# Performance work log

Measured on AMD Instinct MI355X. Metric: run time of the kernel, lower is better.

Reference implementation:

```python
import jax, jax.numpy as jnp
import numpy as np

D_MODEL = 768
N_HEADS = 12
HEAD_DIM = D_MODEL // N_HEADS


def setup_inputs() -> dict:
    key = jax.random.key(0)
    ks = jax.random.split(key, 9)
    B, S = 4, 2048
    std = 1.0 / np.sqrt(D_MODEL)
    x = jax.random.normal(ks[0], (B, S, D_MODEL), dtype=jnp.float32)
    Wq = jax.random.normal(ks[1], (D_MODEL, D_MODEL), dtype=jnp.float32) * std
    bq = jnp.zeros((D_MODEL,), dtype=jnp.float32)
    Wk = jax.random.normal(ks[2], (D_MODEL, D_MODEL), dtype=jnp.float32) * std
    bk = jnp.zeros((D_MODEL,), dtype=jnp.float32)
    Wv = jax.random.normal(ks[3], (D_MODEL, D_MODEL), dtype=jnp.float32) * std
    bv = jnp.zeros((D_MODEL,), dtype=jnp.float32)
    Wo = jax.random.normal(ks[4], (D_MODEL, D_MODEL), dtype=jnp.float32) * std
    bo = jnp.zeros((D_MODEL,), dtype=jnp.float32)
    return {"x": x, "Wq": Wq, "bq": bq, "Wk": Wk, "bk": bk,
            "Wv": Wv, "bv": bv, "Wo": Wo, "bo": bo}


def reference(x, Wq, bq, Wk, bk, Wv, bv, Wo, bo):
    B, S, D = x.shape
    H, Hd = N_HEADS, HEAD_DIM
    # QKV projections (torch Linear: y = x @ W^T + b; here W stored as [in,out])
    q = (x @ Wq + bq).reshape(B, S, H, Hd).transpose(0, 2, 1, 3)  # [B,H,S,Hd]
    k = (x @ Wk + bk).reshape(B, S, H, Hd).transpose(0, 2, 1, 3)
    v = (x @ Wv + bv).reshape(B, S, H, Hd).transpose(0, 2, 1, 3)
    scale = 1.0 / jnp.sqrt(jnp.asarray(Hd, dtype=x.dtype))
    scores = jnp.einsum('bhqd,bhkd->bhqk', q, k) * scale  # [B,H,S,S]
    causal = jnp.tril(jnp.ones((S, S), dtype=bool))
    scores = jnp.where(causal, scores, -jnp.inf)
    attn = jax.nn.softmax(scores, axis=-1)
    ctx = jnp.einsum('bhqk,bhkd->bhqd', attn, v)  # [B,H,S,Hd]
    ctx = ctx.transpose(0, 2, 1, 3).reshape(B, S, D)
    return ctx @ Wo + bo
```

## Files before the change

### kernel.cpp

```cpp
#include <hip/hip_runtime.h>
#include <stdint.h>

#define DM    768
#define NH    12
#define HD    64
#define BATCH 4
#define SEQ   2048
#define NTOK  (BATCH*SEQ)
#define NKT   12

typedef unsigned int   u32;
typedef unsigned short u16;
using bf16x8 = __attribute__((ext_vector_type(8))) short;
using f32x4  = __attribute__((ext_vector_type(4))) float;

#define QSCALE 0.18033688011112042f

__device__ __forceinline__ u16 f2bf(float f) {
    u32 u = __float_as_uint(f);
    u = (u + 0x7FFFu + ((u >> 16) & 1u)) >> 16;
    return (u16)u;
}

__device__ __forceinline__ u32 pkbf(float a, float b) {
    u32 r;
    asm("v_cvt_pk_bf16_f32 %0, %1, %2" : "=v"(r) : "v"(a), "v"(b));
    return r;
}

template <int N>
__device__ __forceinline__ void waitvm() {
    if constexpr (N == 0)      asm volatile("s_waitcnt vmcnt(0)" ::: "memory");
    else if constexpr (N == 5) asm volatile("s_waitcnt vmcnt(5)" ::: "memory");
    else if constexpr (N == 8) asm volatile("s_waitcnt vmcnt(8)" ::: "memory");
    else if constexpr (N == 9) asm volatile("s_waitcnt vmcnt(9)" ::: "memory");
    else                       static_assert(N == 0 || N == 5 || N == 8 || N == 9, "add literal");
}

__device__ __forceinline__ void gload_lds16(const void* gptr, void* ldsptr) {
    __builtin_amdgcn_global_load_lds(
        (__attribute__((address_space(1))) const u32*)gptr,
        (__attribute__((address_space(3))) u32*)ldsptr, 16, 0, 0);
}

__device__ __forceinline__ float vmax4(f32x4 v) {
    return fmaxf(fmaxf(v[0], v[1]), fmaxf(v[2], v[3]));
}

__global__ void cvt_x(const float* __restrict__ x, u16* __restrict__ xb, int n4) {
    int i = blockIdx.x * blockDim.x + threadIdx.x;
    if (i >= n4) return;
    float4 v = ((const float4*)x)[i];
    ushort4 o;
    o.x = f2bf(v.x); o.y = f2bf(v.y); o.z = f2bf(v.z); o.w = f2bf(v.w);
    ((ushort4*)xb)[i] = o;
}

__global__ void transpose_w4(const float* __restrict__ q, const float* __restrict__ k,
                             const float* __restrict__ v, const float* __restrict__ o,
                             u16* __restrict__ Wt, u16* __restrict__ Wto) {
    __shared__ float tile[32][33];
    int z = blockIdx.z;
    const float* W = (z == 0) ? q : (z == 1) ? k : (z == 2) ? v : o;
    u16* D = (z < 3) ? (Wt + (size_t)z * DM * DM) : Wto;
    int tx = threadIdx.x, ty = threadIdx.y;
    int x0 = blockIdx.x * 32, y0 = blockIdx.y * 32;
    #pragma unroll
    for (int i = 0; i < 32; i += 8)
        tile[ty + i][tx] = W[(size_t)(y0 + ty + i) * DM + x0 + tx];
    __syncthreads();
    #pragma unroll
    for (int i = 0; i < 32; i += 8)
        D[(size_t)(x0 + ty + i) * DM + y0 + tx] = f2bf(tile[tx][ty + i]);
}

template <int MODE>
__global__ __launch_bounds__(512, 2)
void gemm_pipe(const u16* __restrict__ A, const u16* __restrict__ Bt,
               const float* __restrict__ b0, const float* __restrict__ b1,
               const float* __restrict__ b2,
               u16* __restrict__ Qo, u16* __restrict__ Ko, u16* __restrict__ Vto,
               float* __restrict__ Out)
{
    constexpr int BM = (MODE == 0) ? 256 : 128;
    constexpr int BN = (MODE == 0) ? 288 : 192;
    constexpr int MF = 4;
    constexpr int NF = (MODE == 0) ? 9 : 3;
    constexpr int AL = BM / 64;
    constexpr int BFULL = (MODE == 0) ? 4 : 3;

    __shared__ u16 As[2][BM][64];
    __shared__ u16 Bs[2][BN][64];

    const int t = threadIdx.x;
    const int w = t >> 6, l = t & 63;
    const int l15 = l & 15, lg = l >> 4;
    const int m0 = blockIdx.x * BM;
    const int n0 = blockIdx.y * BN;
    const int waveM = ((MODE == 0) ? (w >> 1) : (w >> 2)) * 64;
    const int waveN = (MODE == 0) ? (w & 1) * 144 : (w & 3) * 48;

    f32x4 zf = {0.f, 0.f, 0.f, 0.f};
    f32x4 acc[MF][NF];
    #pragma unroll
    for (int i = 0; i < MF; ++i)
        #pragma unroll
        for (int j = 0; j < NF; ++j) acc[i][j] = zf;

    const u16* Arow0 = A  + (size_t)m0 * DM;
    const u16* Brow0 = Bt + (size_t)n0 * DM;

    auto stage = [&](int d, int k0) {
        #pragma unroll
        for (int i = 0; i < AL; ++i) {
            int f = i * 512 + t;
            int row = f >> 3, c = f & 7;
            int gc = c ^ (row & 7);
            gload_lds16(Arow0 + (size_t)row * DM + k0 + gc * 8, &As[d][row][c * 8]);
        }
        #pragma unroll
        for (int i = 0; i < BFULL; ++i) {
            int f = i * 512 + t;
            int row = f >> 3, c = f & 7;
            int gc = c ^ (row & 7);
            gload_lds16(Brow0 + (size_t)row * DM + k0 + gc * 8, &Bs[d][row][c * 8]);
        }
        if constexpr (MODE == 0) {
            if (t < 256) {
                int f = 2048 + t;
                int row = f >> 3, c = f & 7;
                int gc = c ^ (row & 7);
                gload_lds16(Brow0 + (size_t)row * DM + k0 + gc * 8, &Bs[d][row][c * 8]);
            }
        }
    };
    auto wait_tile = [&]() {
        if constexpr (MODE == 0) {
            if (w < 4) waitvm<9>(); else waitvm<8>();
        } else {
            waitvm<5>();
        }
    };
    auto phase = [&](int d, int kk) {
        const int ch = ((kk * 4 + lg) ^ (l15 & 7)) * 8;
        bf16x8 af[MF], bfr[NF];
        #pragma unroll
        for (int m = 0; m < MF; ++m)
            af[m] = *(const bf16x8*)&As[d][waveM + m * 16 + l15][ch];
        #pragma unroll
        for (int n = 0; n < NF; ++n)
            bfr[n] = *(const bf16x8*)&Bs[d][waveN + n * 16 + l15][ch];
        __builtin_amdgcn_s_setprio(1);
        #pragma unroll
        for (int m = 0; m < MF; ++m)
            #pragma unroll
            for (int n = 0; n < NF; ++n)
                acc[m][n] = __builtin_amdgcn_mfma_f32_16x16x32_bf16(af[m], bfr[n], acc[m][n], 0, 0, 0);
        __builtin_amdgcn_s_setprio(0);
    };

    stage(0, 0);
    stage(1, 64);

    for (int tt = 0; tt < NKT - 1; ++tt) {
        const int c = tt & 1;
        wait_tile();
        __builtin_amdgcn_s_barrier();
        __builtin_amdgcn_sched_barrier(0);
        phase(c, 0);
        phase(c, 1);
        __builtin_amdgcn_sched_barrier(0);
        __builtin_amdgcn_s_barrier();
        __builtin_amdgcn_sched_barrier(0);
        if (tt + 2 < NKT) stage(c, (tt + 2) * 64);
    }
    {
        waitvm<0>();
        __builtin_amdgcn_s_barrier();
        __builtin_amdgcn_sched_barrier(0);
        phase((NKT - 1) & 1, 0);
        phase((NKT - 1) & 1, 1);
    }

    if (MODE == 1) {
        #pragma unroll
        for (int m = 0; m < MF; ++m) {
            int grow = m0 + waveM + m * 16 + lg * 4;
            #pragma unroll
            for (int n = 0; n < NF; ++n) {
                int gcol = n0 + waveN + n * 16 + l15;
                float bias = b0[gcol];
                #pragma unroll
                for (int r = 0; r < 4; ++r)
                    Out[(size_t)(grow + r) * DM + gcol] = acc[m][n][r] + bias;
            }
        }
    } else {
        #pragma unroll
        for (int m = 0; m < MF; ++m) {
            int grow = m0 + waveM + m * 16 + lg * 4;
            int bb = grow >> 11, ss = grow & 2047;
            #pragma unroll
            for (int n = 0; n < NF; ++n) {
                int nstart = n0 + waveN + n * 16;
                int which = nstart / DM;
                int cbase = nstart - which * DM + l15;
                int h = cbase >> 6, hd = cbase & 63;
                if (which == 0) {
                    float bias = b0[cbase];
                    #pragma unroll
                    for (int r = 0; r < 4; ++r)
                        Qo[(((size_t)bb * NH + h) * SEQ + (ss + r)) * HD + hd] =
                            f2bf((acc[m][n][r] + bias) * QSCALE);
                } else if (which == 1) {
                    float bias = b1[cbase];
                    #pragma unroll
                    for (int r = 0; r < 4; ++r)
                        Ko[(((size_t)bb * NH + h) * SEQ + (ss + r)) * HD + hd] =
                            f2bf(acc[m][n][r] + bias);
                } else {
                    float bias = b2[cbase];
                    u32 lo = pkbf(acc[m][n][0] + bias, acc[m][n][1] + bias);
                    u32 hi = pkbf(acc[m][n][2] + bias, acc[m][n][3] + bias);
                    *(int2*)&Vto[(((size_t)bb * NH + h) * HD + hd) * SEQ + ss] =
                        make_int2((int)lo, (int)hi);
                }
            }
        }
    }
}

__global__ __launch_bounds__(512, 3)
void attn_fwd(const u16* __restrict__ Q, const u16* __restrict__ K_,
              const u16* __restrict__ Vt, u16* __restrict__ ctx)
{
    __shared__ u16 Ks[2][64][64];
    __shared__ u16 Vs[2][64][64];

    const int t = threadIdx.x, w = t >> 6, l = t & 63;
    const int l15 = l & 15, lg = l >> 4;
    const int sw = l15 & 7;
    const int bx = blockIdx.x;
    const int ord = bx / 48;
    const int bh  = bx - ord * 48;
    const int q8  = 7 - ord;
    const int b = bh / NH, h = bh - b * NH;
    const int wrow0 = q8 * 256 + w * 32;
    const int jmax = 4 * q8 + 3;

    const u16* Qp0 = Q + ((size_t)bh * SEQ + wrow0 + l15) * HD;
    const u16* Qp1 = Qp0 + 16 * HD;
    bf16x8 qf00 = *(const bf16x8*)(Qp0 + lg * 8);
    bf16x8 qf01 = *(const bf16x8*)(Qp0 + 32 + lg * 8);
    bf16x8 qf10 = *(const bf16x8*)(Qp1 + lg * 8);
    bf16x8 qf11 = *(const bf16x8*)(Qp1 + 32 + lg * 8);

    f32x4 zf = {0.f, 0.f, 0.f, 0.f};
    f32x4 acc0[4], acc1[4];
    #pragma unroll
    for (int d = 0; d < 4; ++d) { acc0[d] = zf; acc1[d] = zf; }
    float mi0 = -INFINITY, li0 = 0.f;
    float mi1 = -INFINITY, li1 = 0.f;

    const u16* Kbh = K_ + (size_t)bh * SEQ * HD;
    const u16* Vbh = Vt + (size_t)bh * HD * SEQ;
    const int row = t >> 3, c = t & 7;
    const int cw = (c ^ (row & 7)) * 8;

    {
        int4 kr = *(const int4*)(Kbh + (size_t)row * HD + c * 8);
        int4 vr = *(const int4*)(Vbh + (size_t)row * SEQ + c * 8);
        *(int4*)&Ks[0][row][cw] = kr;
        *(int4*)&Vs[0][row][cw] = vr;
    }
    __syncthreads();

    for (int jt = 0; jt <= jmax; ++jt) {
        const int cur = jt & 1;
        const int j0 = jt << 6;
        int4 kn, vn;
        if (jt < jmax) {
            int j1 = j0 + 64;
            kn = *(const int4*)(Kbh + (size_t)(j1 + row) * HD + c * 8);
            vn = *(const int4*)(Vbh + (size_t)row * SEQ + j1 + c * 8);
        }
        if (j0 <= wrow0 + 31) {
            const u16 (*Kc)[64] = Ks[cur];
            const u16 (*Vc)[64] = Vs[cur];
            f32x4 s0[4], s1[4];
            __builtin_amdgcn_s_setprio(1);
            #pragma unroll
            for (int nt = 0; nt < 4; ++nt) {
                bf16x8 kf0 = *(const bf16x8*)&Kc[nt * 16 + l15][(lg ^ sw) * 8];
                bf16x8 kf1 = *(const bf16x8*)&Kc[nt * 16 + l15][((4 + lg) ^ sw) * 8];
                f32x4 a = zf;
                a = __builtin_amdgcn_mfma_f32_16x16x32_bf16(kf0, qf00, a, 0, 0, 0);
                a = __builtin_amdgcn_mfma_f32_16x16x32_bf16(kf1, qf01, a, 0, 0, 0);
                s0[nt] = a;
                f32x4 c2 = zf;
                c2 = __builtin_amdgcn_mfma_f32_16x16x32_bf16(kf0, qf10, c2, 0, 0, 0);
                c2 = __builtin_amdgcn_mfma_f32_16x16x32_bf16(kf1, qf11, c2, 0, 0, 0);
                s1[nt] = c2;
            }
            __builtin_amdgcn_s_setprio(0);
            if (j0 + 63 > wrow0) {
                #pragma unroll
                for (int nt = 0; nt < 4; ++nt) {
                    int kb = j0 + nt * 16 + lg * 4;
                    #pragma unroll
                    for (int r = 0; r < 4; ++r) {
                        if (kb + r > wrow0 + l15)      s0[nt][r] = -INFINITY;
                        if (kb + r > wrow0 + 16 + l15) s1[nt][r] = -INFINITY;
                    }
                }
            }
            float pm0 = fmaxf(fmaxf(vmax4(s0[0]), vmax4(s0[1])), fmaxf(vmax4(s0[2]), vmax4(s0[3])));
            float pm1 = fmaxf(fmaxf(vmax4(s1[0]), vmax4(s1[1])), fmaxf(vmax4(s1[2]), vmax4(s1[3])));
            pm0 = fmaxf(pm0, __shfl_xor(pm0, 16)); pm0 = fmaxf(pm0, __shfl_xor(pm0, 32));
            pm1 = fmaxf(pm1, __shfl_xor(pm1, 16)); pm1 = fmaxf(pm1, __shfl_xor(pm1, 32));
            if (!__all((pm0 <= mi0 + 8.f) && (pm1 <= mi1 + 8.f))) {
                float mn0 = fmaxf(mi0, pm0), mn1 = fmaxf(mi1, pm1);
                float so0 = __builtin_amdgcn_exp2f(mi0 - mn0);
                float so1 = __builtin_amdgcn_exp2f(mi1 - mn1);
                mi0 = mn0; mi1 = mn1;
                li0 *= so0; li1 *= so1;
                float a0 = __shfl(so0, lg * 4 + 0), a1 = __shfl(so0, lg * 4 + 1);
                float a2 = __shfl(so0, lg * 4 + 2), a3 = __shfl(so0, lg * 4 + 3);
                float b0_ = __shfl(so1, lg * 4 + 0), b1_ = __shfl(so1, lg * 4 + 1);
                float b2_ = __shfl(so1, lg * 4 + 2), b3_ = __shfl(so1, lg * 4 + 3);
                #pragma unroll
                for (int d = 0; d < 4; ++d) {
                    acc0[d][0] *= a0;  acc0[d][1] *= a1;  acc0[d][2] *= a2;  acc0[d][3] *= a3;
                    acc1[d][0] *= b0_; acc1[d][1] *= b1_; acc1[d][2] *= b2_; acc1[d][3] *= b3_;
                }
            }
            u32 dwa[8], dwb[8];
            float rs0 = 0.f, rs1 = 0.f;
            #pragma unroll
            for (int nt = 0; nt < 4; ++nt) {
                float p0 = __builtin_amdgcn_exp2f(s0[nt][0] - mi0);
                float p1 = __builtin_amdgcn_exp2f(s0[nt][1] - mi0);
                float p2 = __builtin_amdgcn_exp2f(s0[nt][2] - mi0);
                float p3 = __builtin_amdgcn_exp2f(s0[nt][3] - mi0);
                rs0 += (p0 + p1) + (p2 + p3);
                dwa[nt * 2] = pkbf(p0, p1); dwa[nt * 2 + 1] = pkbf(p2, p3);
                float q0 = __builtin_amdgcn_exp2f(s1[nt][0] - mi1);
                float q1 = __builtin_amdgcn_exp2f(s1[nt][1] - mi1);
                float q2 = __builtin_amdgcn_exp2f(s1[nt][2] - mi1);
                float q3 = __builtin_amdgcn_exp2f(s1[nt][3] - mi1);
                rs1 += (q0 + q1) + (q2 + q3);
                dwb[nt * 2] = pkbf(q0, q1); dwb[nt * 2 + 1] = pkbf(q2, q3);
            }
            bf16x8 pa00 = __builtin_bit_cast(bf16x8, make_int4((int)dwa[0], (int)dwa[1], (int)dwa[2], (int)dwa[3]));
            bf16x8 pa01 = __builtin_bit_cast(bf16x8, make_int4((int)dwa[4], (int)dwa[5], (int)dwa[6], (int)dwa[7]));
            bf16x8 pa10 = __builtin_bit_cast(bf16x8, make_int4((int)dwb[0], (int)dwb[1], (int)dwb[2], (int)dwb[3]));
            bf16x8 pa11 = __builtin_bit_cast(bf16x8, make_int4((int)dwb[4], (int)dwb[5], (int)dwb[6], (int)dwb[7]));
            const int o4 = (lg & 1) * 4, c0 = lg >> 1;
            __builtin_amdgcn_s_setprio(1);
            #pragma unroll
            for (int d = 0; d < 4; ++d) {
                const u16* vrow = Vc[d * 16 + l15];
                int2 v0 = *(const int2*)(vrow + (((c0 + 0) ^ sw) * 8 + o4));
                int2 v1 = *(const int2*)(vrow + (((c0 + 2) ^ sw) * 8 + o4));
                int2 v2 = *(const int2*)(vrow + (((c0 + 4) ^ sw) * 8 + o4));
                int2 v3 = *(const int2*)(vrow + (((c0 + 6) ^ sw) * 8 + o4));
                bf16x8 vf0 = __builtin_bit_cast(bf16x8, make_int4(v0.x, v0.y, v1.x, v1.y));
                bf16x8 vf1 = __builtin_bit_cast(bf16x8, make_int4(v2.x, v2.y, v3.x, v3.y));
                acc0[d] = __builtin_amdgcn_mfma_f32_16x16x32_bf16(pa00, vf0, acc0[d], 0, 0, 0);
                acc0[d] = __builtin_amdgcn_mfma_f32_16x16x32_bf16(pa01, vf1, acc0[d], 0, 0, 0);
                acc1[d] = __builtin_amdgcn_mfma_f32_16x16x32_bf16(pa10, vf0, acc1[d], 0, 0, 0);
                acc1[d] = __builtin_amdgcn_mfma_f32_16x16x32_bf16(pa11, vf1, acc1[d], 0, 0, 0);
            }
            __builtin_amdgcn_s_setprio(0);
            rs0 += __shfl_xor(rs0, 16); rs0 += __shfl_xor(rs0, 32);
            rs1 += __shfl_xor(rs1, 16); rs1 += __shfl_xor(rs1, 32);
            li0 += rs0; li1 += rs1;
        }
        if (jt < jmax) {
            *(int4*)&Ks[cur ^ 1][row][cw] = kn;
            *(int4*)&Vs[cur ^ 1][row][cw] = vn;
        }
        __syncthreads();
    }

    float e00 = 1.0f / __shfl(li0, lg * 4 + 0), e01 = 1.0f / __shfl(li0, lg * 4 + 1);
    float e02 = 1.0f / __shfl(li0, lg * 4 + 2), e03 = 1.0f / __shfl(li0, lg * 4 + 3);
    float e10 = 1.0f / __shfl(li1, lg * 4 + 0), e11 = 1.0f / __shfl(li1, lg * 4 + 1);
    float e12 = 1.0f / __shfl(li1, lg * 4 + 2), e13 = 1.0f / __shfl(li1, lg * 4 + 3);
    #pragma unroll
    for (int r = 0; r < 4; ++r) {
        float f0 = (r == 0) ? e00 : (r == 1) ? e01 : (r == 2) ? e02 : e03;
        float f1 = (r == 0) ? e10 : (r == 1) ? e11 : (r == 2) ? e12 : e13;
        int s0r = wrow0 + lg * 4 + r;
        size_t base0 = ((size_t)b * SEQ + s0r) * DM + h * HD;
        size_t base1 = ((size_t)b * SEQ + s0r + 16) * DM + h * HD;
        #pragma unroll
        for (int d = 0; d < 4; ++d) {
            ctx[base0 + d * 16 + l15] = f2bf(acc0[d][r] * f0);
            ctx[base1 + d * 16 + l15] = f2bf(acc1[d][r] * f1);
        }
    }
}

extern "C" void kernel_launch(void* const* d_in, const int* in_sizes, int n_in,
                              void* d_out, int out_size, void* d_ws, size_t ws_size,
                              hipStream_t stream) {
    const float* x  = (const float*)d_in[0];
    const float* Wq = (const float*)d_in[1];
    const float* bq = (const float*)d_in[2];
    const float* Wk = (const float*)d_in[3];
    const float* bk = (const float*)d_in[4];
    const float* Wv = (const float*)d_in[5];
    const float* bv = (const float*)d_in[6];
    const float* Wo = (const float*)d_in[7];
    const float* bo = (const float*)d_in[8];
    float* out = (float*)d_out;

    char* ws = (char*)d_ws;
    u16* xb  = (u16*)(ws);
    u16* Wt  = (u16*)(ws + 12582912);
    u16* Wto = (u16*)(ws + 16121856);
    u16* Qw  = (u16*)(ws + 17301504);
    u16* Kw  = (u16*)(ws + 29884416);
    u16* Vtw = (u16*)(ws + 42467328);
    u16* ctx = (u16*)(ws + 55050240);

    cvt_x<<<6144, 256, 0, stream>>>(x, xb, NTOK * DM / 4);
    dim3 tb(32, 8), tg4(24, 24, 4);
    transpose_w4<<<tg4, tb, 0, stream>>>(Wq, Wk, Wv, Wo, Wt, Wto);

    dim3 g2(32, 8);
    gemm_pipe<0><<<g2, 512, 0, stream>>>(xb, Wt, bq, bk, bv, Qw, Kw, Vtw, nullptr);
    attn_fwd<<<384, 512, 0, stream>>>(Qw, Kw, Vtw, ctx);
    dim3 g4(64, 4);
    gemm_pipe<1><<<g4, 512, 0, stream>>>(ctx, Wto, bo, nullptr, nullptr, nullptr, nullptr, nullptr, out);
}
```

Before: 135.0 us.

## Double attention KV tile to 128 keys per sync and raise launch bounds

The attention loop now stages 128 keys of K and V per iteration instead of 64. It processes them as two 64-key halves from the same shared buffers, which halves the number of block barriers and global-to-LDS prefetch rounds. The V layout becomes 64x128 with a matching swizzle. Launch bounds rise from 3 to 4 blocks per CU, which tightens the register budget. Shared memory per block doubles to 64KB, which may cap resident blocks below the requested 4 and risks spills or lower occupancy.

Result: slower. 152.3 us (+12.8%).

```diff
diff --git a/kernel.cpp b/kernel.cpp
--- a/kernel.cpp
+++ b/kernel.cpp
@@ -230,12 +230,12 @@
     }
 }
 
-__global__ __launch_bounds__(512, 3)
+__global__ __launch_bounds__(512, 4)
 void attn_fwd(const u16* __restrict__ Q, const u16* __restrict__ K_,
               const u16* __restrict__ Vt, u16* __restrict__ ctx)
 {
-    __shared__ u16 Ks[2][64][64];
-    __shared__ u16 Vs[2][64][64];
+    __shared__ u16 Ks[2][128][64];
+    __shared__ u16 Vs[2][64][128];
 
     const int t = threadIdx.x, w = t >> 6, l = t & 63;
     const int l15 = l & 15, lg = l >> 4;
@@ -246,7 +246,7 @@
     const int q8  = 7 - ord;
     const int b = bh / NH, h = bh - b * NH;
     const int wrow0 = q8 * 256 + w * 32;
-    const int jmax = 4 * q8 + 3;
+    const int niter = 2 * q8 + 2;
 
     const u16* Qp0 = Q + ((size_t)bh * SEQ + wrow0 + l15) * HD;
     const u16* Qp1 = Qp0 + 16 * HD;
@@ -264,121 +264,138 @@
 
     const u16* Kbh = K_ + (size_t)bh * SEQ * HD;
     const u16* Vbh = Vt + (size_t)bh * HD * SEQ;
-    const int row = t >> 3, c = t & 7;
-    const int cw = (c ^ (row & 7)) * 8;
+    const int rk = t >> 3, ck = t & 7;
+    const int rv = t >> 4, cv = t & 15;
+    const int kw0 = (ck ^ (rk & 7)) * 8;
+    const int kw1 = (ck ^ ((rk + 64) & 7)) * 8;
+    const int vw0 = ((cv ^ (rv & 7)) & 15) * 8;
+    const int vw1 = ((cv ^ ((rv + 32) & 7)) & 15) * 8;
 
     {
-        int4 kr = *(const int4*)(Kbh + (size_t)row * HD + c * 8);
-        int4 vr = *(const int4*)(Vbh + (size_t)row * SEQ + c * 8);
-        *(int4*)&Ks[0][row][cw] = kr;
-        *(int4*)&Vs[0][row][cw] = vr;
+        int4 k0r = *(const int4*)(Kbh + (size_t)rk * HD + ck * 8);
+        int4 k1r = *(const int4*)(Kbh + (size_t)(rk + 64) * HD + ck * 8);
+        int4 v0r = *(const int4*)(Vbh + (size_t)rv * SEQ + cv * 8);
+        int4 v1r = *(const int4*)(Vbh + (size_t)(rv + 32) * SEQ + cv * 8);
+        *(int4*)&Ks[0][rk][kw0]      = k0r;
+        *(int4*)&Ks[0][rk + 64][kw1] = k1r;
+        *(int4*)&Vs[0][rv][vw0]      = v0r;
+        *(int4*)&Vs[0][rv + 32][vw1] = v1r;
     }
     __syncthreads();
 
-    for (int jt = 0; jt <= jmax; ++jt) {
+    for (int jt = 0; jt < niter; ++jt) {
         const int cur = jt & 1;
-        const int j0 = jt << 6;
-        int4 kn, vn;
-        if (jt < jmax) {
-            int j1 = j0 + 64;
-            kn = *(const int4*)(Kbh + (size_t)(j1 + row) * HD + c * 8);
-            vn = *(const int4*)(Vbh + (size_t)row * SEQ + j1 + c * 8);
-        }
-        if (j0 <= wrow0 + 31) {
-            const u16 (*Kc)[64] = Ks[cur];
-            const u16 (*Vc)[64] = Vs[cur];
-            f32x4 s0[4], s1[4];
-            __builtin_amdgcn_s_setprio(1);
-            #pragma unroll
-            for (int nt = 0; nt < 4; ++nt) {
-                bf16x8 kf0 = *(const bf16x8*)&Kc[nt * 16 + l15][(lg ^ sw) * 8];
-                bf16x8 kf1 = *(const bf16x8*)&Kc[nt * 16 + l15][((4 + lg) ^ sw) * 8];
-                f32x4 a = zf;
-                a = __builtin_amdgcn_mfma_f32_16x16x32_bf16(kf0, qf00, a, 0, 0, 0);
-                a = __builtin_amdgcn_mfma_f32_16x16x32_bf16(kf1, qf01, a, 0, 0, 0);
-                s0[nt] = a;
-                f32x4 c2 = zf;
-                c2 = __builtin_amdgcn_mfma_f32_16x16x32_bf16(kf0, qf10, c2, 0, 0, 0);
-                c2 = __builtin_amdgcn_mfma_f32_16x16x32_bf16(kf1, qf11, c2, 0, 0, 0);
-                s1[nt] = c2;
-            }
-            __builtin_amdgcn_s_setprio(0);
-            if (j0 + 63 > wrow0) {
+        const int j0 = jt << 7;
+        int4 kn0, kn1, vn0, vn1;
+        if (jt < niter - 1) {
+            int j1 = j0 + 128;
+            kn0 = *(const int4*)(Kbh + (size_t)(j1 + rk) * HD + ck * 8);
+            kn1 = *(const int4*)(Kbh + (size_t)(j1 + rk + 64) * HD + ck * 8);
+            vn0 = *(const int4*)(Vbh + (size_t)rv * SEQ + j1 + cv * 8);
+            vn1 = *(const int4*)(Vbh + (size_t)(rv + 32) * SEQ + j1 + cv * 8);
+        }
+        const u16 (*Kc)[64]  = Ks[cur];
+        const u16 (*Vc)[128] = Vs[cur];
+        #pragma unroll
+        for (int hk = 0; hk < 2; ++hk) {
+            const int j0h = j0 + hk * 64;
+            if (j0h <= wrow0 + 31) {
+                f32x4 s0[4], s1[4];
+                __builtin_amdgcn_s_setprio(1);
                 #pragma unroll
                 for (int nt = 0; nt < 4; ++nt) {
-                    int kb = j0 + nt * 16 + lg * 4;
+                    const u16* krow = Kc[hk * 64 + nt * 16 + l15];
+                    bf16x8 kf0 = *(const bf16x8*)&krow[(lg ^ sw) * 8];
+                    bf16x8 kf1 = *(const bf16x8*)&krow[((4 + lg) ^ sw) * 8];
+                    f32x4 a = zf;
+                    a = __builtin_amdgcn_mfma_f32_16x16x32_bf16(kf0, qf00, a, 0, 0, 0);
+                    a = __builtin_amdgcn_mfma_f32_16x16x32_bf16(kf1, qf01, a, 0, 0, 0);
+                    s0[nt] = a;
+                    f32x4 c2 = zf;
+                    c2 = __builtin_amdgcn_mfma_f32_16x16x32_bf16(kf0, qf10, c2, 0, 0, 0);
+                    c2 = __builtin_amdgcn_mfma_f32_16x16x32_bf16(kf1, qf11, c2, 0, 0, 0);
+                    s1[nt] = c2;
+                }
+                __builtin_amdgcn_s_setprio(0);
+                if (j0h + 63 > wrow0) {
                     #pragma unroll
-                    for (int r = 0; r < 4; ++r) {
-                        if (kb + r > wrow0 + l15)      s0[nt][r] = -INFINITY;
-                        if (kb + r > wrow0 + 16 + l15) s1[nt][r] = -INFINITY;
+                    for (int nt = 0; nt < 4; ++nt) {
+                        int kb = j0h + nt * 16 + lg * 4;
+                        #pragma unroll
+                        for (int r = 0; r < 4; ++r) {
+                            if (kb + r > wrow0 + l15)      s0[nt][r] = -INFINITY;
+                            if (kb + r > wrow0 + 16 + l15) s1[nt][r] = -INFINITY;
+                        }
                     }
                 }
-            }
-            float pm0 = fmaxf(fmaxf(vmax4(s0[0]), vmax4(s0[1])), fmaxf(vmax4(s0[2]), vmax4(s0[3])));
-            float pm1 = fmaxf(fmaxf(vmax4(s1[0]), vmax4(s1[1])), fmaxf(vmax4(s1[2]), vmax4(s1[3])));
-            pm0 = fmaxf(pm0, __shfl_xor(pm0, 16)); pm0 = fmaxf(pm0, __shfl_xor(pm0, 32));
-            pm1 = fmaxf(pm1, __shfl_xor(pm1, 16)); pm1 = fmaxf(pm1, __shfl_xor(pm1, 32));
-            if (!__all((pm0 <= mi0 + 8.f) && (pm1 <= mi1 + 8.f))) {
-                float mn0 = fmaxf(mi0, pm0), mn1 = fmaxf(mi1, pm1);
-                float so0 = __builtin_amdgcn_exp2f(mi0 - mn0);
-                float so1 = __builtin_amdgcn_exp2f(mi1 - mn1);
-                mi0 = mn0; mi1 = mn1;
-                li0 *= so0; li1 *= so1;
-                float a0 = __shfl(so0, lg * 4 + 0), a1 = __shfl(so0, lg * 4 + 1);
-                float a2 = __shfl(so0, lg * 4 + 2), a3 = __shfl(so0, lg * 4 + 3);
-                float b0_ = __shfl(so1, lg * 4 + 0), b1_ = __shfl(so1, lg * 4 + 1);
-                float b2_ = __shfl(so1, lg * 4 + 2), b3_ = __shfl(so1, lg * 4 + 3);
+                float pm0 = fmaxf(fmaxf(vmax4(s0[0]), vmax4(s0[1])), fmaxf(vmax4(s0[2]), vmax4(s0[3])));
+                float pm1 = fmaxf(fmaxf(vmax4(s1[0]), vmax4(s1[1])), fmaxf(vmax4(s1[2]), vmax4(s1[3])));
+                pm0 = fmaxf(pm0, __shfl_xor(pm0, 16)); pm0 = fmaxf(pm0, __shfl_xor(pm0, 32));
+                pm1 = fmaxf(pm1, __shfl_xor(pm1, 16)); pm1 = fmaxf(pm1, __shfl_xor(pm1, 32));
+                if (!__all((pm0 <= mi0 + 8.f) && (pm1 <= mi1 + 8.f))) {
+                    float mn0 = fmaxf(mi0, pm0), mn1 = fmaxf(mi1, pm1);
+                    float so0 = __builtin_amdgcn_exp2f(mi0 - mn0);
+                    float so1 = __builtin_amdgcn_exp2f(mi1 - mn1);
+                    mi0 = mn0; mi1 = mn1;
+                    li0 *= so0; li1 *= so1;
+                    float a0 = __shfl(so0, lg * 4 + 0), a1 = __shfl(so0, lg * 4 + 1);
+                    float a2 = __shfl(so0, lg * 4 + 2), a3 = __shfl(so0, lg * 4 + 3);
+                    float b0_ = __shfl(so1, lg * 4 + 0), b1_ = __shfl(so1, lg * 4 + 1);
+                    float b2_ = __shfl(so1, lg * 4 + 2), b3_ = __shfl(so1, lg * 4 + 3);
+                    #pragma unroll
+                    for (int d = 0; d < 4; ++d) {
+                        acc0[d][0] *= a0;  acc0[d][1] *= a1;  acc0[d][2] *= a2;  acc0[d][3] *= a3;
+                        acc1[d][0] *= b0_; acc1[d][1] *= b1_; acc1[d][2] *= b2_; acc1[d][3] *= b3_;
+                    }
+                }
+                u32 dwa[8], dwb[8];
+                float rs0 = 0.f, rs1 = 0.f;
+                #pragma unroll
+                for (int nt = 0; nt < 4; ++nt) {
+                    float p0 = __builtin_amdgcn_exp2f(s0[nt][0] - mi0);
+                    float p1 = __builtin_amdgcn_exp2f(s0[nt][1] - mi0);
+                    float p2 = __builtin_amdgcn_exp2f(s0[nt][2] - mi0);
+                    float p3 = __builtin_amdgcn_exp2f(s0[nt][3] - mi0);
+                    rs0 += (p0 + p1) + (p2 + p3);
+                    dwa[nt * 2] = pkbf(p0, p1); dwa[nt * 2 + 1] = pkbf(p2, p3);
+                    float q0 = __builtin_amdgcn_exp2f(s1[nt][0] - mi1);
+                    float q1 = __builtin_amdgcn_exp2f(s1[nt][1] - mi1);
+                    float q2 = __builtin_amdgcn_exp2f(s1[nt][2] - mi1);
+                    float q3 = __builtin_amdgcn_exp2f(s1[nt][3] - mi1);
+                    rs1 += (q0 + q1) + (q2 + q3);
+                    dwb[nt * 2] = pkbf(q0, q1); dwb[nt * 2 + 1] = pkbf(q2, q3);
+                }
+                rs0 += __shfl_xor(rs0, 16); rs0 += __shfl_xor(rs0, 32);
+                rs1 += __shfl_xor(rs1, 16); rs1 += __shfl_xor(rs1, 32);
+                li0 += rs0; li1 += rs1;
+                bf16x8 pa00 = __builtin_bit_cast(bf16x8, make_int4((int)dwa[0], (int)dwa[1], (int)dwa[2], (int)dwa[3]));
+                bf16x8 pa01 = __builtin_bit_cast(bf16x8, make_int4((int)dwa[4], (int)dwa[5], (int)dwa[6], (int)dwa[7]));
+                bf16x8 pa10 = __builtin_bit_cast(bf16x8, make_int4((int)dwb[0], (int)dwb[1], (int)dwb[2], (int)dwb[3]));
+                bf16x8 pa11 = __builtin_bit_cast(bf16x8, make_int4((int)dwb[4], (int)dwb[5], (int)dwb[6], (int)dwb[7]));
+                const int o4 = (lg & 1) * 4, c0 = lg >> 1;
+                __builtin_amdgcn_s_setprio(1);
                 #pragma unroll
                 for (int d = 0; d < 4; ++d) {
-                    acc0[d][0] *= a0;  acc0[d][1] *= a1;  acc0[d][2] *= a2;  acc0[d][3] *= a3;
-                    acc1[d][0] *= b0_; acc1[d][1] *= b1_; acc1[d][2] *= b2_; acc1[d][3] *= b3_;
-                }
+                    const u16* vrow = Vc[d * 16 + l15] + hk * 64;
+                    int2 v0 = *(const int2*)(vrow + (((c0 + 0) ^ sw) * 8 + o4));
+                    int2 v1 = *(const int2*)(vrow + (((c0 + 2) ^ sw) * 8 + o4));
+                    int2 v2 = *(const int2*)(vrow + (((c0 + 4) ^ sw) * 8 + o4));
+                    int2 v3 = *(const int2*)(vrow + (((c0 + 6) ^ sw) * 8 + o4));
+                    bf16x8 vf0 = __builtin_bit_cast(bf16x8, make_int4(v0.x, v0.y, v1.x, v1.y));
+                    bf16x8 vf1 = __builtin_bit_cast(bf16x8, make_int4(v2.x, v2.y, v3.x, v3.y));
+                    acc0[d] = __builtin_amdgcn_mfma_f32_16x16x32_bf16(pa00, vf0, acc0[d], 0, 0, 0);
+                    acc0[d] = __builtin_amdgcn_mfma_f32_16x16x32_bf16(pa01, vf1, acc0[d], 0, 0, 0);
+                    acc1[d] = __builtin_amdgcn_mfma_f32_16x16x32_bf16(pa10, vf0, acc1[d], 0, 0, 0);
+                    acc1[d] = __builtin_amdgcn_mfma_f32_16x16x32_bf16(pa11, vf1, acc1[d], 0, 0, 0);
+                }
+                __builtin_amdgcn_s_setprio(0);
             }
-            u32 dwa[8], dwb[8];
-            float rs0 = 0.f, rs1 = 0.f;
-            #pragma unroll
-            for (int nt = 0; nt < 4; ++nt) {
-                float p0 = __builtin_amdgcn_exp2f(s0[nt][0] - mi0);
-                float p1 = __builtin_amdgcn_exp2f(s0[nt][1] - mi0);
-                float p2 = __builtin_amdgcn_exp2f(s0[nt][2] - mi0);
-                float p3 = __builtin_amdgcn_exp2f(s0[nt][3] - mi0);
-                rs0 += (p0 + p1) + (p2 + p3);
-                dwa[nt * 2] = pkbf(p0, p1); dwa[nt * 2 + 1] = pkbf(p2, p3);
-                float q0 = __builtin_amdgcn_exp2f(s1[nt][0] - mi1);
-                float q1 = __builtin_amdgcn_exp2f(s1[nt][1] - mi1);
-                float q2 = __builtin_amdgcn_exp2f(s1[nt][2] - mi1);
-                float q3 = __builtin_amdgcn_exp2f(s1[nt][3] - mi1);
-                rs1 += (q0 + q1) + (q2 + q3);
-                dwb[nt * 2] = pkbf(q0, q1); dwb[nt * 2 + 1] = pkbf(q2, q3);
-            }
-            bf16x8 pa00 = __builtin_bit_cast(bf16x8, make_int4((int)dwa[0], (int)dwa[1], (int)dwa[2], (int)dwa[3]));
-            bf16x8 pa01 = __builtin_bit_cast(bf16x8, make_int4((int)dwa[4], (int)dwa[5], (int)dwa[6], (int)dwa[7]));
-            bf16x8 pa10 = __builtin_bit_cast(bf16x8, make_int4((int)dwb[0], (int)dwb[1], (int)dwb[2], (int)dwb[3]));
-            bf16x8 pa11 = __builtin_bit_cast(bf16x8, make_int4((int)dwb[4], (int)dwb[5], (int)dwb[6], (int)dwb[7]));
-            const int o4 = (lg & 1) * 4, c0 = lg >> 1;
-            __builtin_amdgcn_s_setprio(1);
-            #pragma unroll
-            for (int d = 0; d < 4; ++d) {
-                const u16* vrow = Vc[d * 16 + l15];
-                int2 v0 = *(const int2*)(vrow + (((c0 + 0) ^ sw) * 8 + o4));
-                int2 v1 = *(const int2*)(vrow + (((c0 + 2) ^ sw) * 8 + o4));
-                int2 v2 = *(const int2*)(vrow + (((c0 + 4) ^ sw) * 8 + o4));
-                int2 v3 = *(const int2*)(vrow + (((c0 + 6) ^ sw) * 8 + o4));
-                bf16x8 vf0 = __builtin_bit_cast(bf16x8, make_int4(v0.x, v0.y, v1.x, v1.y));
-                bf16x8 vf1 = __builtin_bit_cast(bf16x8, make_int4(v2.x, v2.y, v3.x, v3.y));
-                acc0[d] = __builtin_amdgcn_mfma_f32_16x16x32_bf16(pa00, vf0, acc0[d], 0, 0, 0);
-                acc0[d] = __builtin_amdgcn_mfma_f32_16x16x32_bf16(pa01, vf1, acc0[d], 0, 0, 0);
-                acc1[d] = __builtin_amdgcn_mfma_f32_16x16x32_bf16(pa10, vf0, acc1[d], 0, 0, 0);
-                acc1[d] = __builtin_amdgcn_mfma_f32_16x16x32_bf16(pa11, vf1, acc1[d], 0, 0, 0);
-            }
-            __builtin_amdgcn_s_setprio(0);
-            rs0 += __shfl_xor(rs0, 16); rs0 += __shfl_xor(rs0, 32);
-            rs1 += __shfl_xor(rs1, 16); rs1 += __shfl_xor(rs1, 32);
-            li0 += rs0; li1 += rs1;
-        }
-        if (jt < jmax) {
-            *(int4*)&Ks[cur ^ 1][row][cw] = kn;
-            *(int4*)&Vs[cur ^ 1][row][cw] = vn;
+        }
+        if (jt < niter - 1) {
+            *(int4*)&Ks[cur ^ 1][rk][kw0]      = kn0;
+            *(int4*)&Ks[cur ^ 1][rk + 64][kw1] = kn1;
+            *(int4*)&Vs[cur ^ 1][rv][vw0]      = vn0;
+            *(int4*)&Vs[cur ^ 1][rv + 32][vw1] = vn1;
         }
         __syncthreads();
     }
```
